# Kernel tuning notes

Measured on AMD Instinct MI355X. Metric: run time of the kernel, lower is better.

The kernel has to match this reference:

```python
import jax, jax.numpy as jnp
import numpy as np

B, L, D = 64, 2048, 256
T_CLAIM, T_PREM = 16, 32
NEG = jnp.float32(-1e9)


def setup_inputs() -> dict:
    key = jax.random.key(0)
    ks = jax.random.split(key, 40)
    f32 = jnp.float32

    def n(k, shape, scale):
        return jax.random.normal(k, shape, f32) * scale

    inp = {}
    inp["sentence_feat"] = n(ks[0], (B, L, D), 1.0)
    inp["sentence_mask"] = jnp.ones((B, L), jnp.int32)
    inp["gold_claim_head"] = jax.random.randint(ks[1], (B, T_CLAIM), 0, L, jnp.int32)
    inp["gold_premise_head"] = jax.random.randint(ks[2], (B, T_PREM), 0, L, jnp.int32)
    inp["query_claim"] = n(ks[3], (D,), 1.0)
    inp["query_premise"] = n(ks[4], (D,), 1.0)
    s = D ** -0.5
    for px, kb in (("c_", 5), ("p_", 20)):
        inp[px + "bil_W"] = n(ks[kb + 0], (D, D, D), 1.0 / D)   # (out,in1,in2)
        inp[px + "bil_b"] = jnp.zeros((D,), f32)
        inp[px + "Wq"] = n(ks[kb + 1], (D, D), s)
        inp[px + "Wk"] = n(ks[kb + 2], (D, D), s)
        inp[px + "attn_b"] = jnp.zeros((D,), f32)
        inp[px + "attn_v"] = n(ks[kb + 3], (D,), s)
        inp[px + "Wih"] = n(ks[kb + 4], (3 * D, D), s)
        inp[px + "Whh"] = n(ks[kb + 5], (3 * D, D), s)
        inp[px + "bih"] = jnp.zeros((3 * D,), f32)
        inp[px + "bhh"] = jnp.zeros((3 * D,), f32)
    return inp


def _gru_cell(x, h, Wih, Whh, bih, bhh):
    # torch.nn.GRUCell math
    gi = x @ Wih.T + bih
    gh = h @ Whh.T + bhh
    ir, iz, in_ = jnp.split(gi, 3, axis=-1)
    hr, hz, hn = jnp.split(gh, 3, axis=-1)
    r = jax.nn.sigmoid(ir + hr)
    z = jax.nn.sigmoid(iz + hz)
    nn_ = jnp.tanh(in_ + r * hn)
    return (1.0 - z) * nn_ + z * h


def _pointer_network(parent, sib0, emb, mask, gold,
                     bil_W, bil_b, Wq, Wk, attn_b, attn_v, Wih, Whh, bih, bhh):
    """parent (B,D), sib0 (B,D), emb (B,L,D), mask (B,L), gold (B,T) -> (B,T) gold probs."""
    bidx = jnp.arange(parent.shape[0])
    proj_k = jnp.einsum('bld,de->ble', emb, Wk)  # key projection hoisted out of loop
    valid = mask != 0

    def step(sib, gold_t):
        # bilinear query: q_k = parent W_k sib + b_k
        q = jnp.einsum('bd,kde,be->bk', parent, bil_W, sib) + bil_b  # (B,D)
        h = jnp.tanh(proj_k + (q @ Wq + attn_b)[:, None, :])          # (B,L,D)
        scores = jnp.einsum('bld,d->bl', h, attn_v)                   # (B,L)
        prob = jax.nn.softmax(jnp.where(valid, scores, NEG), axis=-1)
        tp = prob[bidx, gold_t]                                       # gather gold prob
        x = emb[bidx, gold_t]                                         # gather gold embedding
        return _gru_cell(x, sib, Wih, Whh, bih, bhh), tp

    _, probs = jax.lax.scan(step, sib0, gold.T)  # (T,B)
    return probs.T


def reference(sentence_feat, query_claim, query_premise,
              c_bil_W, c_bil_b, c_Wq, c_Wk, c_attn_b, c_attn_v, c_Wih, c_Whh, c_bih, c_bhh,
              p_bil_W, p_bil_b, p_Wq, p_Wk, p_attn_b, p_attn_v, p_Wih, p_Whh, p_bih, p_bhh,
              sentence_mask, gold_claim_head, gold_premise_head):
    global_feat = sentence_feat[:, -2]                       # (B,D)
    sib_c = jnp.broadcast_to(query_claim, global_feat.shape)
    sib_p = jnp.broadcast_to(query_premise, global_feat.shape)
    claim = _pointer_network(global_feat, sib_c, sentence_feat, sentence_mask, gold_claim_head,
                             c_bil_W, c_bil_b, c_Wq, c_Wk, c_attn_b, c_attn_v, c_Wih, c_Whh, c_bih, c_bhh)
    prem = _pointer_network(global_feat, sib_p, sentence_feat, sentence_mask, gold_premise_head,
                            p_bil_W, p_bil_b, p_Wq, p_Wk, p_attn_b, p_attn_v, p_Wih, p_Whh, p_bih, p_bhh)
    return claim, prem
```

## Files before the change

kernel.cpp:

```cpp
#include <hip/hip_runtime.h>
#include <hip/hip_fp16.h>

#define B_ 64
#define L_ 2048
#define D_ 256
#define TC 16
#define TP 32

typedef _Float16 half8 __attribute__((ext_vector_type(8)));
typedef _Float16 f16x2 __attribute__((ext_vector_type(2)));
typedef float f32x4 __attribute__((ext_vector_type(4)));

#define LOG2E 1.4426950408889634f
#define TWO_LOG2E 2.8853900817779268f

__device__ __forceinline__ float ex2(float x){ return __builtin_amdgcn_exp2f(x); }
__device__ __forceinline__ float rcp_(float x){ return __builtin_amdgcn_rcpf(x); }
__device__ __forceinline__ float sigm(float x){ return rcp_(1.f + ex2(-LOG2E*x)); }
__device__ __forceinline__ float tanh_(float x){ return 1.f - 2.f*rcp_(1.f + ex2(TWO_LOG2E*x)); }

#if __has_builtin(__builtin_amdgcn_fdot2)
__device__ __forceinline__ float fdot2_(f16x2 a, f16x2 b, float c){ return __builtin_amdgcn_fdot2(a,b,c,false); }
#else
__device__ __forceinline__ float fdot2_(f16x2 a, f16x2 b, float c){
  return fmaf((float)a[0], (float)b[0], fmaf((float)a[1], (float)b[1], c));
}
#endif

__device__ __forceinline__ void cvt8(uint4 v, float* w){
  const __half2* h = (const __half2*)&v;
#pragma unroll
  for (int i=0;i<4;i++){ float2 f = __half22float2(h[i]); w[2*i]=f.x; w[2*i+1]=f.y; }
}

__global__ __launch_bounds__(256) void k_prep(
    const float* __restrict__ sf,
    const float* __restrict__ wk_c, const float* __restrict__ wk_p,
    const float* __restrict__ wih_c, const float* __restrict__ wih_p,
    const float* __restrict__ whh_c, const float* __restrict__ whh_p,
    __half* __restrict__ wkT, __half* __restrict__ wihH, __half* __restrict__ whhH,
    float* __restrict__ parentT)
{
  int idx = blockIdx.x*256 + threadIdx.x;
  if (idx < 131072) {
    int c = idx >> 8, d = idx & 255;
    int net = c >> 8, e = c & 255;
    const float* w = net ? wk_p : wk_c;
    wkT[idx] = __float2half(w[d*256 + e]);
  } else if (idx < 131072 + 393216) {
    int i = idx - 131072;
    const float* w = (i < 196608) ? wih_c : wih_p;
    wihH[i] = __float2half(w[(i < 196608) ? i : i - 196608]);
  } else if (idx < 131072 + 786432) {
    int i = idx - 131072 - 393216;
    const float* w = (i < 196608) ? whh_c : whh_p;
    whhH[i] = __float2half(w[(i < 196608) ? i : i - 196608]);
  } else {
    int i = idx - 131072 - 786432;
    int d = i >> 6, b = i & 63;
    parentT[i] = sf[((size_t)b*L_ + (L_-2))*D_ + d];
  }
}

__global__ __launch_bounds__(256) void k_gemm(
    const float* __restrict__ sf, const __half* __restrict__ wkT, __half* __restrict__ Eo)
{
  __shared__ __half As[128*40];
  __shared__ __half Bs[128*40];
  const int tid = threadIdx.x;
  const int bid = blockIdx.x;
  const int xcd = bid & 7;
  const int w_  = bid >> 3;
  const int row0 = (xcd*128 + (w_ >> 2)) * 128;
  const int col0 = (w_ & 3) * 128;
  const int lane = tid & 63, wave = tid >> 6;
  const int wm = wave & 1, wn = wave >> 1;
  const int qd = lane >> 4, mr = lane & 15;
  const int rl = tid >> 1, hf = tid & 1;

  f32x4 acc[4][4];
#pragma unroll
  for (int i=0;i<4;i++)
#pragma unroll
    for (int j=0;j<4;j++) acc[i][j] = (f32x4){0.f,0.f,0.f,0.f};

  for (int kc = 0; kc < 256; kc += 32) {
    const float* asrc = sf + ((size_t)(row0+rl))*256 + kc + hf*16;
    __half* adst = As + rl*40 + hf*16;
#pragma unroll
    for (int i=0;i<4;i++){
      float4 v = ((const float4*)asrc)[i];
      __half2 h01 = __floats2half2_rn(v.x, v.y);
      __half2 h23 = __floats2half2_rn(v.z, v.w);
      uint2 u; u.x = *(const unsigned*)&h01; u.y = *(const unsigned*)&h23;
      *(uint2*)(adst + i*4) = u;
    }
    const __half* bsrc = wkT + (size_t)(col0+rl)*256 + kc + hf*16;
    __half* bdst = Bs + rl*40 + hf*16;
    *(uint4*)bdst       = *(const uint4*)bsrc;
    *(uint4*)(bdst + 8) = *(const uint4*)(bsrc + 8);
    __syncthreads();

    half8 af[4], bf[4];
#pragma unroll
    for (int tm=0;tm<4;tm++) af[tm] = *(const half8*)(As + (wm*64 + tm*16 + mr)*40 + qd*8);
#pragma unroll
    for (int tn=0;tn<4;tn++) bf[tn] = *(const half8*)(Bs + (wn*64 + tn*16 + mr)*40 + qd*8);
#pragma unroll
    for (int tm=0;tm<4;tm++)
#pragma unroll
      for (int tn=0;tn<4;tn++)
        acc[tm][tn] = __builtin_amdgcn_mfma_f32_16x16x32_f16(af[tm], bf[tn], acc[tm][tn], 0,0,0);
    __syncthreads();
  }
#pragma unroll
  for (int tm=0;tm<4;tm++)
#pragma unroll
    for (int tn=0;tn<4;tn++){
      int c = col0 + wn*64 + tn*16 + mr;
#pragma unroll
      for (int rg=0; rg<4; rg++){
        int r = row0 + wm*64 + tm*16 + qd*4 + rg;
        float e = ex2(TWO_LOG2E * acc[tm][tn][rg]);
        Eo[(size_t)r*512 + c] = __float2half(fminf(e, 65000.f));
      }
    }
}

__global__ __launch_bounds__(256) void k_M(
    const float* __restrict__ bw_c, const float* __restrict__ bw_p,
    const float* __restrict__ parentT, float* __restrict__ M)
{
  const int net = blockIdx.x >> 8;
  const int k = blockIdx.x & 255;
  const int e = threadIdx.x;
  __shared__ float pl[16384];
#pragma unroll
  for (int r=0;r<16;r++){
    int f4 = r*256 + threadIdx.x;
    ((float4*)pl)[f4] = ((const float4*)parentT)[f4];
  }
  __syncthreads();

  const float* W = (net ? bw_p : bw_c) + (size_t)k*65536 + e;
  float acc[64];
#pragma unroll
  for (int b=0;b<64;b++) acc[b] = 0.f;
  float wcur = W[0];
  for (int d=0; d<256; d++){
    float wnext = (d < 255) ? W[(size_t)(d+1)*256] : 0.f;
    const float4* pr = (const float4*)(pl + d*64);
#pragma unroll
    for (int c=0;c<16;c++){
      float4 pv = pr[c];
      acc[c*4+0] = fmaf(pv.x, wcur, acc[c*4+0]);
      acc[c*4+1] = fmaf(pv.y, wcur, acc[c*4+1]);
      acc[c*4+2] = fmaf(pv.z, wcur, acc[c*4+2]);
      acc[c*4+3] = fmaf(pv.w, wcur, acc[c*4+3]);
    }
    wcur = wnext;
  }
  float* Mo = M + ((size_t)net*64*256 + k)*256 + e;
#pragma unroll
  for (int b=0;b<64;b++) Mo[(size_t)b*65536] = acc[b];
}

template<int T>
__global__ __launch_bounds__(256) void k_gi(
    const float* __restrict__ sf, const int* __restrict__ gold,
    const __half* __restrict__ wih, const float* __restrict__ bih,
    float* __restrict__ gi_all)
{
  const int jc = blockIdx.x % 3;
  const int bb = blockIdx.x / 3;
  __shared__ float xs[T-1][256];
  const int* gr = gold + bb*T;
  for (int t=0; t<T-1; t++)
    xs[t][threadIdx.x] = sf[((size_t)bb*L_ + gr[t])*D_ + threadIdx.x];
  __syncthreads();
  const int j = jc*256 + threadIdx.x;
  const __half* wr = wih + (size_t)j*256;
  float acc[T-1];
#pragma unroll
  for (int t=0;t<T-1;t++) acc[t] = 0.f;
  for (int d0=0; d0<256; d0+=8){
    uint4 wv = *(const uint4*)(wr + d0);
    float w[8]; cvt8(wv, w);
#pragma unroll
    for (int t=0;t<T-1;t++){
      const float* xr = &xs[t][d0];
      float4 a = *(const float4*)xr;
      float4 b = *(const float4*)(xr+4);
      acc[t] += w[0]*a.x + w[1]*a.y + w[2]*a.z + w[3]*a.w
              + w[4]*b.x + w[5]*b.y + w[6]*b.z + w[7]*b.w;
    }
  }
  float bias = bih[j];
  float* go = gi_all + ((size_t)bb*32)*768 + j;
#pragma unroll
  for (int t=0;t<T-1;t++) go[(size_t)t*768] = acc[t] + bias;
}

__global__ __launch_bounds__(768, 3) void k_gru(
    const float* __restrict__ query_c, const float* __restrict__ query_p,
    const __half* __restrict__ whhH,
    const float* __restrict__ bhh_c, const float* __restrict__ bhh_p,
    const float* __restrict__ gi_all, float* __restrict__ sibT)
{
  const int net = blockIdx.x >> 6, bb = blockIdx.x & 63;
  const int T = net ? TP : TC;
  const int j = threadIdx.x;
  __shared__ float hs[256];
  __shared__ __half hsh[256];
  __shared__ float gh[768];
  const __half* wr = whhH + (size_t)net*196608 + (size_t)j*256;
  const float bias = (net ? bhh_p : bhh_c)[j];
  const float* gir = gi_all + (size_t)(net*64+bb)*32*768;
  float* sib = sibT + (size_t)(net*64+bb)*256*32;
  const float* query = net ? query_p : query_c;

  uint4 wreg[32];
#pragma unroll
  for (int i=0;i<32;i++) wreg[i] = ((const uint4*)wr)[i];

  if (j < 256){ float h0 = query[j]; hs[j]=h0; hsh[j]=__float2half(h0); sib[j*32]=h0; }
  __syncthreads();
  for (int t=0; t<T-1; t++){
    float a0 = bias, a1 = 0.f, a2 = 0.f, a3 = 0.f;
#pragma unroll
    for (int i=0;i<32;i+=4){
      uint4 hv0 = ((const uint4*)hsh)[i+0];
      uint4 hv1 = ((const uint4*)hsh)[i+1];
      uint4 hv2 = ((const uint4*)hsh)[i+2];
      uint4 hv3 = ((const uint4*)hsh)[i+3];
      const f16x2* wp0 = (const f16x2*)&wreg[i+0]; const f16x2* hp0 = (const f16x2*)&hv0;
      const f16x2* wp1 = (const f16x2*)&wreg[i+1]; const f16x2* hp1 = (const f16x2*)&hv1;
      const f16x2* wp2 = (const f16x2*)&wreg[i+2]; const f16x2* hp2 = (const f16x2*)&hv2;
      const f16x2* wp3 = (const f16x2*)&wreg[i+3]; const f16x2* hp3 = (const f16x2*)&hv3;
#pragma unroll
      for (int i2=0;i2<4;i2++){
        a0 = fdot2_(wp0[i2], hp0[i2], a0);
        a1 = fdot2_(wp1[i2], hp1[i2], a1);
        a2 = fdot2_(wp2[i2], hp2[i2], a2);
        a3 = fdot2_(wp3[i2], hp3[i2], a3);
      }
    }
    gh[j] = (a0 + a1) + (a2 + a3);
    __syncthreads();
    if (j < 256){
      const float* gi = gir + (size_t)t*768;
      float r = sigm(gi[j] + gh[j]);
      float z = sigm(gi[256+j] + gh[256+j]);
      float n = tanh_(gi[512+j] + r*gh[512+j]);
      float hn = (1.f - z)*n + z*hs[j];
      hs[j] = hn; hsh[j] = __float2half(hn);
      sib[j*32 + t + 1] = hn;
    }
    __syncthreads();
  }
}

__global__ __launch_bounds__(256) void k_qt(
    const float* __restrict__ M, const float* __restrict__ sibT,
    const float* __restrict__ bb_c, const float* __restrict__ bb_p,
    const float* __restrict__ wq_c, const float* __restrict__ wq_p,
    const float* __restrict__ ab_c, const float* __restrict__ ab_p,
    float* __restrict__ Qo)
{
  const int bb = blockIdx.x;
  const int y = blockIdx.y;
  const int net = (y >= 2) ? 1 : 0;
  const int t0 = net ? (y-2)*8 : y*8;
  const int tid = threadIdx.x;
  __shared__ float qs[256][8];
  __shared__ float slds[256][8];

  {
    const float* sr = sibT + ((size_t)(net*64+bb))*256*32 + t0;
#pragma unroll
    for (int r=0;r<2;r++){
      int f4 = r*256 + tid;
      int e = f4 >> 1, hh = f4 & 1;
      *(float4*)&slds[e][hh*4] = *(const float4*)(sr + (size_t)e*32 + hh*4);
    }
  }
  __syncthreads();

  const float* Mr = M + (((size_t)(net*64+bb))*256 + tid)*256;
  float accq[8];
  const float b0 = (net ? bb_p : bb_c)[tid];
#pragma unroll
  for (int t=0;t<8;t++) accq[t] = b0;
  for (int e0=0; e0<256; e0+=4){
    float4 m4 = *(const float4*)(Mr + e0);
#pragma unroll
    for (int ee=0; ee<4; ee++){
      float4 sa = *(const float4*)&slds[e0+ee][0];
      float4 sb = *(const float4*)&slds[e0+ee][4];
      float mv = ((const float*)&m4)[ee];
      accq[0] = fmaf(mv, sa.x, accq[0]); accq[1] = fmaf(mv, sa.y, accq[1]);
      accq[2] = fmaf(mv, sa.z, accq[2]); accq[3] = fmaf(mv, sa.w, accq[3]);
      accq[4] = fmaf(mv, sb.x, accq[4]); accq[5] = fmaf(mv, sb.y, accq[5]);
      accq[6] = fmaf(mv, sb.z, accq[6]); accq[7] = fmaf(mv, sb.w, accq[7]);
    }
  }
#pragma unroll
  for (int t=0;t<8;t++) qs[tid][t] = accq[t];
  __syncthreads();

  const float* wq = (net ? wq_p : wq_c) + tid;
  float acc2[8];
  const float a0 = (net ? ab_p : ab_c)[tid];
#pragma unroll
  for (int t=0;t<8;t++) acc2[t] = a0;
  for (int k=0; k<256; k++){
    float w = wq[(size_t)k*256];
#pragma unroll
    for (int t=0;t<8;t++) acc2[t] = fmaf(qs[k][t], w, acc2[t]);
  }
  float* qo = Qo + (((size_t)(net*64+bb))*256 + tid)*32 + t0;
#pragma unroll
  for (int t=0;t<8;t++) qo[t] = fminf(ex2(TWO_LOG2E * acc2[t]), 3.0e4f);
}

__global__ __launch_bounds__(256) void k_fused(
    const __half* __restrict__ E, const float* __restrict__ Q,
    const float* __restrict__ av_c, const float* __restrict__ av_p,
    const int* __restrict__ mask,
    const int* __restrict__ gold_c, const int* __restrict__ gold_p,
    float* __restrict__ partials, float* __restrict__ gold_e)
{
  const int bb = blockIdx.x;
  const int lc = blockIdx.y;
  const int nc = blockIdx.z;
  const int net = nc ? 1 : 0;
  const int t0 = (nc == 2) ? 16 : 0;
  const int l  = lc*256 + threadIdx.x;
  const __half* pr = E + ((size_t)bb*L_ + l)*512 + net*256;
  const float* qr = Q + ((size_t)(net*64+bb))*256*32 + t0;
  const float* av = net ? av_p : av_c;

  float acc[16];
#pragma unroll
  for (int t=0;t<16;t++) acc[t] = 0.f;

  for (int d0=0; d0<256; d0+=8){
    uint4 pv = *(const uint4*)(pr + d0);
    float x[8]; cvt8(pv, x);
#pragma unroll
    for (int h=0; h<2; h++){
      const int d = d0 + h*4;
      const float v0 = av[d+0], v1 = av[d+1], v2 = av[d+2], v3 = av[d+3];
      const float xa = x[h*4+0], xb = x[h*4+1], xc = x[h*4+2], xd = x[h*4+3];
      const float* q0p = qr + (size_t)(d+0)*32;
      const float* q1p = qr + (size_t)(d+1)*32;
      const float* q2p = qr + (size_t)(d+2)*32;
      const float* q3p = qr + (size_t)(d+3)*32;
#pragma unroll
      for (int tc=0; tc<16; tc+=4){
        float4 qa  = *(const float4*)(q0p + tc);
        float4 qb  = *(const float4*)(q1p + tc);
        float4 qc  = *(const float4*)(q2p + tc);
        float4 qd4 = *(const float4*)(q3p + tc);
        const float qas[4] = {qa.x, qa.y, qa.z, qa.w};
        const float qbs[4] = {qb.x, qb.y, qb.z, qb.w};
        const float qcs[4] = {qc.x, qc.y, qc.z, qc.w};
        const float qds[4] = {qd4.x,qd4.y,qd4.z,qd4.w};
#pragma unroll
        for (int tt=0; tt<4; tt++){
          float ta = fmaf(xa, qas[tt], 1.f);
          float tb = fmaf(xb, qbs[tt], 1.f);
          float tcv= fmaf(xc, qcs[tt], 1.f);
          float td = fmaf(xd, qds[tt], 1.f);
          float t01 = ta*tb, t23 = tcv*td;
          float n01 = fmaf(v0, tb, v1*ta);
          float n23 = fmaf(v2, td, v3*tcv);
          float num = fmaf(n01, t23, n23*t01);
          float den = t01*t23;
          acc[tc+tt] = fmaf(num, rcp_(den), acc[tc+tt]);
        }
      }
    }
  }

  const int m = mask[bb*L_ + l];
  float ex[16];
#pragma unroll
  for (int t=0;t<16;t++) ex[t] = m ? ex2(-TWO_LOG2E * acc[t]) : 0.f;

  const int* g = net ? (gold_p + bb*TP + t0) : (gold_c + bb*TC);
#pragma unroll
  for (int t=0;t<16;t++)
    if (l == g[t]) gold_e[net*2048 + bb*32 + t0 + t] = ex[t];

#pragma unroll
  for (int off=1; off<64; off<<=1)
#pragma unroll
    for (int t=0;t<16;t++) ex[t] += __shfl_xor(ex[t], off, 64);

  __shared__ float red4[4][16];
  const int lane = threadIdx.x & 63, wave = threadIdx.x >> 6;
  if (lane == 0)
#pragma unroll
    for (int t=0;t<16;t++) red4[wave][t] = ex[t];
  __syncthreads();
  if (threadIdx.x < 16){
    float s = red4[0][threadIdx.x] + red4[1][threadIdx.x]
            + red4[2][threadIdx.x] + red4[3][threadIdx.x];
    partials[(((size_t)nc*64 + bb)*8 + lc)*16 + threadIdx.x] = s;
  }
}

__global__ __launch_bounds__(256) void k_fin(
    const float* __restrict__ partials, const float* __restrict__ gold_e,
    float* __restrict__ out)
{
  int id = blockIdx.x*256 + threadIdx.x;
  if (id >= 3072) return;
  int net, bb, t, nc, tt;
  if (id < 1024){ net=0; bb=id>>4; t=id&15; nc=0; tt=t; }
  else { int i=id-1024; net=1; bb=i>>5; t=i&31; nc=1+(t>>4); tt=t&15; }
  const float* pr = partials + (((size_t)nc*64 + bb)*8)*16 + tt;
  float s = 0.f;
#pragma unroll
  for (int lcx=0; lcx<8; lcx++) s += pr[lcx*16];
  out[net ? (1024 + bb*TP + t) : (bb*TC + t)] = gold_e[net*2048 + bb*32 + t] / s;
}

extern "C" void kernel_launch(void* const* d_in, const int* in_sizes, int n_in,
                              void* d_out, int out_size, void* d_ws, size_t ws_size,
                              hipStream_t stream)
{
  const float* sf      = (const float*)d_in[0];
  const int*   mask    = (const int*)d_in[1];
  const int*   gold_c  = (const int*)d_in[2];
  const int*   gold_p  = (const int*)d_in[3];
  const float* query_c = (const float*)d_in[4];
  const float* query_p = (const float*)d_in[5];
  const float* c_bw  = (const float*)d_in[6];
  const float* c_bb  = (const float*)d_in[7];
  const float* c_wq  = (const float*)d_in[8];
  const float* c_wk  = (const float*)d_in[9];
  const float* c_ab  = (const float*)d_in[10];
  const float* c_av  = (const float*)d_in[11];
  const float* c_wih = (const float*)d_in[12];
  const float* c_whh = (const float*)d_in[13];
  const float* c_bih = (const float*)d_in[14];
  const float* c_bhh = (const float*)d_in[15];
  const float* p_bw  = (const float*)d_in[16];
  const float* p_bb  = (const float*)d_in[17];
  const float* p_wq  = (const float*)d_in[18];
  const float* p_wk  = (const float*)d_in[19];
  const float* p_ab  = (const float*)d_in[20];
  const float* p_av  = (const float*)d_in[21];
  const float* p_wih = (const float*)d_in[22];
  const float* p_whh = (const float*)d_in[23];
  const float* p_bih = (const float*)d_in[24];
  const float* p_bhh = (const float*)d_in[25];
  float* out = (float*)d_out;

  char* w = (char*)d_ws;
  size_t o = 0;
  auto take = [&](size_t bytes){ char* p = w + o; o += (bytes + 255) & ~(size_t)255; return p; };
  __half* E      = (__half*)take((size_t)131072*512*2);
  float*  M      = (float*) take((size_t)2*64*256*256*4);
  float*  Q      = (float*) take((size_t)2*64*256*32*4);
  float*  sibT   = (float*) take((size_t)2*64*256*32*4);
  float*  gi_all = (float*) take((size_t)2*64*32*768*4);
  float*  partials=(float*) take((size_t)3*64*8*16*4);
  float*  gold_e = (float*) take((size_t)2*64*32*4);
  __half* wkT    = (__half*)take((size_t)512*256*2);
  __half* wihH   = (__half*)take((size_t)2*768*256*2);
  __half* whhH   = (__half*)take((size_t)2*768*256*2);
  float*  parentT= (float*) take((size_t)256*64*4);
  (void)ws_size; (void)in_sizes; (void)n_in; (void)out_size;

  k_prep<<<3648, 256, 0, stream>>>(sf, c_wk, p_wk, c_wih, p_wih, c_whh, p_whh,
                                   wkT, wihH, whhH, parentT);
  k_gemm<<<4096, 256, 0, stream>>>(sf, wkT, E);
  k_M<<<512, 256, 0, stream>>>(c_bw, p_bw, parentT, M);
  k_gi<TC><<<192, 256, 0, stream>>>(sf, gold_c, wihH,          c_bih, gi_all);
  k_gi<TP><<<192, 256, 0, stream>>>(sf, gold_p, wihH + 196608, p_bih, gi_all + (size_t)64*32*768);
  k_gru<<<128, 768, 0, stream>>>(query_c, query_p, whhH, c_bhh, p_bhh, gi_all, sibT);
  k_qt<<<dim3(64,6), 256, 0, stream>>>(M, sibT, c_bb, p_bb, c_wq, p_wq, c_ab, p_ab, Q);
  k_fused<<<dim3(64,8,3), 256, 0, stream>>>(E, Q, c_av, p_av, mask, gold_c, gold_p,
                                            partials, gold_e);
  k_fin<<<12, 256, 0, stream>>>(partials, gold_e, out);
}
```

Baseline: 763.0 us.

## Merge M/gi kernels, drop Wih fp16 conversion, restructure premise scoring split

Merges the bilinear M kernel and both GRU input-gate kernels into one launch, and removes the Wih fp16 conversion so gi reads fp32 weights directly. Rewrites the scoring kernel so each premise thread covers all 32 timesteps over half of D, with the two halves combined through shared memory. This reuses each loaded E element across twice as many timesteps, and the E loads are software-prefetched. The cost is higher register pressure (32 accumulators plus the ex array) and an extra block-level reduction.

```diff
diff --git a/kernel.cpp b/kernel.cpp
--- a/kernel.cpp
+++ b/kernel.cpp
@@ -33,12 +33,51 @@
   for (int i=0;i<4;i++){ float2 f = __half22float2(h[i]); w[2*i]=f.x; w[2*i+1]=f.y; }
 }
 
+template<int NT>
+__device__ __forceinline__ void octet_body(const float* x, const float* av_d,
+                                           const float* qr_d, float* acc)
+{
+#pragma unroll
+  for (int h=0; h<2; h++){
+    const int d = h*4;
+    const float v0 = av_d[d+0], v1 = av_d[d+1], v2 = av_d[d+2], v3 = av_d[d+3];
+    const float xa = x[h*4+0], xb = x[h*4+1], xc = x[h*4+2], xd = x[h*4+3];
+    const float* q0p = qr_d + (size_t)(d+0)*32;
+    const float* q1p = qr_d + (size_t)(d+1)*32;
+    const float* q2p = qr_d + (size_t)(d+2)*32;
+    const float* q3p = qr_d + (size_t)(d+3)*32;
+#pragma unroll
+    for (int tc=0; tc<NT; tc+=4){
+      float4 qa  = *(const float4*)(q0p + tc);
+      float4 qb  = *(const float4*)(q1p + tc);
+      float4 qc  = *(const float4*)(q2p + tc);
+      float4 qd4 = *(const float4*)(q3p + tc);
+      const float qas[4] = {qa.x, qa.y, qa.z, qa.w};
+      const float qbs[4] = {qb.x, qb.y, qb.z, qb.w};
+      const float qcs[4] = {qc.x, qc.y, qc.z, qc.w};
+      const float qds[4] = {qd4.x,qd4.y,qd4.z,qd4.w};
+#pragma unroll
+      for (int tt=0; tt<4; tt++){
+        float ta = fmaf(xa, qas[tt], 1.f);
+        float tb = fmaf(xb, qbs[tt], 1.f);
+        float tcv= fmaf(xc, qcs[tt], 1.f);
+        float td = fmaf(xd, qds[tt], 1.f);
+        float t01 = ta*tb, t23 = tcv*td;
+        float n01 = fmaf(v0, tb, v1*ta);
+        float n23 = fmaf(v2, td, v3*tcv);
+        float num = fmaf(n01, t23, n23*t01);
+        float den = t01*t23;
+        acc[tc+tt] = fmaf(num, rcp_(den), acc[tc+tt]);
+      }
+    }
+  }
+}
+
 __global__ __launch_bounds__(256) void k_prep(
     const float* __restrict__ sf,
     const float* __restrict__ wk_c, const float* __restrict__ wk_p,
-    const float* __restrict__ wih_c, const float* __restrict__ wih_p,
     const float* __restrict__ whh_c, const float* __restrict__ whh_p,
-    __half* __restrict__ wkT, __half* __restrict__ wihH, __half* __restrict__ whhH,
+    __half* __restrict__ wkT, __half* __restrict__ whhH,
     float* __restrict__ parentT)
 {
   int idx = blockIdx.x*256 + threadIdx.x;
@@ -49,14 +88,10 @@
     wkT[idx] = __float2half(w[d*256 + e]);
   } else if (idx < 131072 + 393216) {
     int i = idx - 131072;
-    const float* w = (i < 196608) ? wih_c : wih_p;
-    wihH[i] = __float2half(w[(i < 196608) ? i : i - 196608]);
-  } else if (idx < 131072 + 786432) {
-    int i = idx - 131072 - 393216;
     const float* w = (i < 196608) ? whh_c : whh_p;
     whhH[i] = __float2half(w[(i < 196608) ? i : i - 196608]);
   } else {
-    int i = idx - 131072 - 786432;
+    int i = idx - 524288;
     int d = i >> 6, b = i & 63;
     parentT[i] = sf[((size_t)b*L_ + (L_-2))*D_ + d];
   }
@@ -127,65 +162,27 @@
     }
 }
 
-__global__ __launch_bounds__(256) void k_M(
-    const float* __restrict__ bw_c, const float* __restrict__ bw_p,
-    const float* __restrict__ parentT, float* __restrict__ M)
-{
-  const int net = blockIdx.x >> 8;
-  const int k = blockIdx.x & 255;
-  const int e = threadIdx.x;
-  __shared__ float pl[16384];
-#pragma unroll
-  for (int r=0;r<16;r++){
-    int f4 = r*256 + threadIdx.x;
-    ((float4*)pl)[f4] = ((const float4*)parentT)[f4];
-  }
-  __syncthreads();
-
-  const float* W = (net ? bw_p : bw_c) + (size_t)k*65536 + e;
-  float acc[64];
-#pragma unroll
-  for (int b=0;b<64;b++) acc[b] = 0.f;
-  float wcur = W[0];
-  for (int d=0; d<256; d++){
-    float wnext = (d < 255) ? W[(size_t)(d+1)*256] : 0.f;
-    const float4* pr = (const float4*)(pl + d*64);
-#pragma unroll
-    for (int c=0;c<16;c++){
-      float4 pv = pr[c];
-      acc[c*4+0] = fmaf(pv.x, wcur, acc[c*4+0]);
-      acc[c*4+1] = fmaf(pv.y, wcur, acc[c*4+1]);
-      acc[c*4+2] = fmaf(pv.z, wcur, acc[c*4+2]);
-      acc[c*4+3] = fmaf(pv.w, wcur, acc[c*4+3]);
-    }
-    wcur = wnext;
-  }
-  float* Mo = M + ((size_t)net*64*256 + k)*256 + e;
-#pragma unroll
-  for (int b=0;b<64;b++) Mo[(size_t)b*65536] = acc[b];
-}
-
 template<int T>
-__global__ __launch_bounds__(256) void k_gi(
-    const float* __restrict__ sf, const int* __restrict__ gold,
-    const __half* __restrict__ wih, const float* __restrict__ bih,
-    float* __restrict__ gi_all)
-{
-  const int jc = blockIdx.x % 3;
-  const int bb = blockIdx.x / 3;
-  __shared__ float xs[T-1][256];
+__device__ void gi_body(const float* __restrict__ sf, const int* __restrict__ gold,
+                        const float* __restrict__ wih, const float* __restrict__ bih,
+                        float* __restrict__ gi_out, int idx, float* xsm)
+{
+  const int jc = idx % 3;
+  const int bb = idx / 3;
+  float (*xs)[256] = (float(*)[256])xsm;
   const int* gr = gold + bb*T;
   for (int t=0; t<T-1; t++)
     xs[t][threadIdx.x] = sf[((size_t)bb*L_ + gr[t])*D_ + threadIdx.x];
   __syncthreads();
   const int j = jc*256 + threadIdx.x;
-  const __half* wr = wih + (size_t)j*256;
+  const float* wr = wih + (size_t)j*256;
   float acc[T-1];
 #pragma unroll
   for (int t=0;t<T-1;t++) acc[t] = 0.f;
   for (int d0=0; d0<256; d0+=8){
-    uint4 wv = *(const uint4*)(wr + d0);
-    float w[8]; cvt8(wv, w);
+    float4 wa = *(const float4*)(wr + d0);
+    float4 wb = *(const float4*)(wr + d0 + 4);
+    const float w[8] = {wa.x,wa.y,wa.z,wa.w, wb.x,wb.y,wb.z,wb.w};
 #pragma unroll
     for (int t=0;t<T-1;t++){
       const float* xr = &xs[t][d0];
@@ -196,9 +193,60 @@
     }
   }
   float bias = bih[j];
-  float* go = gi_all + ((size_t)bb*32)*768 + j;
+  float* go = gi_out + ((size_t)bb*32)*768 + j;
 #pragma unroll
   for (int t=0;t<T-1;t++) go[(size_t)t*768] = acc[t] + bias;
+}
+
+__global__ __launch_bounds__(256) void k_Mgi(
+    const float* __restrict__ bw_c, const float* __restrict__ bw_p,
+    const float* __restrict__ parentT, float* __restrict__ M,
+    const float* __restrict__ sf,
+    const int* __restrict__ gold_c, const int* __restrict__ gold_p,
+    const float* __restrict__ wih_c, const float* __restrict__ wih_p,
+    const float* __restrict__ bih_c, const float* __restrict__ bih_p,
+    float* __restrict__ gi_all)
+{
+  __shared__ float smem[16384];
+  const int bid = blockIdx.x;
+  if (bid < 512) {
+    const int net = bid >> 8;
+    const int k = bid & 255;
+    const int e = threadIdx.x;
+    float* pl = smem;
+#pragma unroll
+    for (int r=0;r<16;r++){
+      int f4 = r*256 + threadIdx.x;
+      ((float4*)pl)[f4] = ((const float4*)parentT)[f4];
+    }
+    __syncthreads();
+
+    const float* W = (net ? bw_p : bw_c) + (size_t)k*65536 + e;
+    float acc[64];
+#pragma unroll
+    for (int b=0;b<64;b++) acc[b] = 0.f;
+    float wcur = W[0];
+    for (int d=0; d<256; d++){
+      float wnext = (d < 255) ? W[(size_t)(d+1)*256] : 0.f;
+      const float4* pr = (const float4*)(pl + d*64);
+#pragma unroll
+      for (int c=0;c<16;c++){
+        float4 pv = pr[c];
+        acc[c*4+0] = fmaf(pv.x, wcur, acc[c*4+0]);
+        acc[c*4+1] = fmaf(pv.y, wcur, acc[c*4+1]);
+        acc[c*4+2] = fmaf(pv.z, wcur, acc[c*4+2]);
+        acc[c*4+3] = fmaf(pv.w, wcur, acc[c*4+3]);
+      }
+      wcur = wnext;
+    }
+    float* Mo = M + ((size_t)net*64*256 + k)*256 + e;
+#pragma unroll
+    for (int b=0;b<64;b++) Mo[(size_t)b*65536] = acc[b];
+  } else if (bid < 704) {
+    gi_body<TC>(sf, gold_c, wih_c, bih_c, gi_all, bid-512, smem);
+  } else {
+    gi_body<TP>(sf, gold_p, wih_p, bih_p, gi_all + (size_t)64*32*768, bid-704, smem);
+  }
 }
 
 __global__ __launch_bounds__(768, 3) void k_gru(
@@ -323,108 +371,147 @@
   for (int t=0;t<8;t++) qo[t] = fminf(ex2(TWO_LOG2E * acc2[t]), 3.0e4f);
 }
 
-__global__ __launch_bounds__(256) void k_fused(
+__global__ __launch_bounds__(256) void k_fused2(
     const __half* __restrict__ E, const float* __restrict__ Q,
     const float* __restrict__ av_c, const float* __restrict__ av_p,
     const int* __restrict__ mask,
     const int* __restrict__ gold_c, const int* __restrict__ gold_p,
-    float* __restrict__ partials, float* __restrict__ gold_e)
+    float* __restrict__ partials_c, float* __restrict__ partials_p,
+    float* __restrict__ gold_e)
 {
   const int bb = blockIdx.x;
-  const int lc = blockIdx.y;
-  const int nc = blockIdx.z;
-  const int net = nc ? 1 : 0;
-  const int t0 = (nc == 2) ? 16 : 0;
-  const int l  = lc*256 + threadIdx.x;
-  const __half* pr = E + ((size_t)bb*L_ + l)*512 + net*256;
-  const float* qr = Q + ((size_t)(net*64+bb))*256*32 + t0;
-  const float* av = net ? av_p : av_c;
-
-  float acc[16];
-#pragma unroll
-  for (int t=0;t<16;t++) acc[t] = 0.f;
-
-  for (int d0=0; d0<256; d0+=8){
-    uint4 pv = *(const uint4*)(pr + d0);
-    float x[8]; cvt8(pv, x);
-#pragma unroll
-    for (int h=0; h<2; h++){
-      const int d = d0 + h*4;
-      const float v0 = av[d+0], v1 = av[d+1], v2 = av[d+2], v3 = av[d+3];
-      const float xa = x[h*4+0], xb = x[h*4+1], xc = x[h*4+2], xd = x[h*4+3];
-      const float* q0p = qr + (size_t)(d+0)*32;
-      const float* q1p = qr + (size_t)(d+1)*32;
-      const float* q2p = qr + (size_t)(d+2)*32;
-      const float* q3p = qr + (size_t)(d+3)*32;
-#pragma unroll
-      for (int tc=0; tc<16; tc+=4){
-        float4 qa  = *(const float4*)(q0p + tc);
-        float4 qb  = *(const float4*)(q1p + tc);
-        float4 qc  = *(const float4*)(q2p + tc);
-        float4 qd4 = *(const float4*)(q3p + tc);
-        const float qas[4] = {qa.x, qa.y, qa.z, qa.w};
-        const float qbs[4] = {qb.x, qb.y, qb.z, qb.w};
-        const float qcs[4] = {qc.x, qc.y, qc.z, qc.w};
-        const float qds[4] = {qd4.x,qd4.y,qd4.z,qd4.w};
-#pragma unroll
-        for (int tt=0; tt<4; tt++){
-          float ta = fmaf(xa, qas[tt], 1.f);
-          float tb = fmaf(xb, qbs[tt], 1.f);
-          float tcv= fmaf(xc, qcs[tt], 1.f);
-          float td = fmaf(xd, qds[tt], 1.f);
-          float t01 = ta*tb, t23 = tcv*td;
-          float n01 = fmaf(v0, tb, v1*ta);
-          float n23 = fmaf(v2, td, v3*tcv);
-          float num = fmaf(n01, t23, n23*t01);
-          float den = t01*t23;
-          acc[tc+tt] = fmaf(num, rcp_(den), acc[tc+tt]);
-        }
+  const int y  = blockIdx.y;
+  const int tid = threadIdx.x;
+  const int lane = tid & 63, wave = tid >> 6;
+  __shared__ float redP[128][32];
+  __shared__ float red2[2][32];
+
+  if (y < 8) {
+    const int lc = y;
+    const int l  = lc*256 + tid;
+    const __half* pr = E + ((size_t)bb*L_ + l)*512;
+    const float* qr = Q + ((size_t)bb)*256*32;
+    const float* av = av_c;
+
+    float acc[16];
+#pragma unroll
+    for (int t=0;t<16;t++) acc[t] = 0.f;
+
+    const uint4* e4 = (const uint4*)pr;
+    uint4 pv = e4[0];
+    for (int o=0; o<32; o++){
+      uint4 nx = e4[(o<31)?(o+1):31];
+      float x[8]; cvt8(pv, x);
+      const int d0 = o*8;
+      octet_body<16>(x, av + d0, qr + (size_t)d0*32, acc);
+      pv = nx;
+    }
+
+    const int m = mask[bb*L_ + l];
+    float ex[16];
+#pragma unroll
+    for (int t=0;t<16;t++) ex[t] = m ? ex2(-TWO_LOG2E * acc[t]) : 0.f;
+
+    const int* g = gold_c + bb*TC;
+#pragma unroll
+    for (int t=0;t<16;t++)
+      if (l == g[t]) gold_e[bb*32 + t] = ex[t];
+
+#pragma unroll
+    for (int off=1; off<64; off<<=1)
+#pragma unroll
+      for (int t=0;t<16;t++) ex[t] += __shfl_xor(ex[t], off, 64);
+
+    if (lane == 0)
+#pragma unroll
+      for (int t=0;t<16;t++) redP[wave][t] = ex[t];
+    __syncthreads();
+    if (tid < 16){
+      float s = redP[0][tid] + redP[1][tid] + redP[2][tid] + redP[3][tid];
+      partials_c[((size_t)bb*8 + lc)*16 + tid] = s;
+    }
+  } else {
+    const int lc = y - 8;
+    const int lloc = tid & 127, hh = tid >> 7;
+    const int l = lc*128 + lloc;
+    const __half* pr = E + ((size_t)bb*L_ + l)*512 + 256 + hh*128;
+    const float* qr = Q + ((size_t)(64+bb)*256 + hh*128)*32;
+    const float* av = av_p + hh*128;
+
+    float acc[32];
+#pragma unroll
+    for (int t=0;t<32;t++) acc[t] = 0.f;
+
+    const uint4* e4 = (const uint4*)pr;
+    uint4 pv = e4[0];
+    for (int o=0; o<16; o++){
+      uint4 nx = e4[(o<15)?(o+1):15];
+      float x[8]; cvt8(pv, x);
+      const int d0 = o*8;
+      octet_body<32>(x, av + d0, qr + (size_t)d0*32, acc);
+      pv = nx;
+    }
+
+    if (hh == 1){
+#pragma unroll
+      for (int t=0;t<32;t++) redP[lloc][t] = acc[t];
+    }
+    __syncthreads();
+
+    float ex[32];
+#pragma unroll
+    for (int t=0;t<32;t++) ex[t] = 0.f;
+    if (hh == 0){
+      const int m = mask[bb*L_ + l];
+      const int* g = gold_p + bb*TP;
+#pragma unroll
+      for (int t=0;t<32;t++){
+        float a = acc[t] + redP[lloc][t];
+        ex[t] = m ? ex2(-TWO_LOG2E * a) : 0.f;
       }
-    }
-  }
-
-  const int m = mask[bb*L_ + l];
-  float ex[16];
-#pragma unroll
-  for (int t=0;t<16;t++) ex[t] = m ? ex2(-TWO_LOG2E * acc[t]) : 0.f;
-
-  const int* g = net ? (gold_p + bb*TP + t0) : (gold_c + bb*TC);
-#pragma unroll
-  for (int t=0;t<16;t++)
-    if (l == g[t]) gold_e[net*2048 + bb*32 + t0 + t] = ex[t];
-
-#pragma unroll
-  for (int off=1; off<64; off<<=1)
-#pragma unroll
-    for (int t=0;t<16;t++) ex[t] += __shfl_xor(ex[t], off, 64);
-
-  __shared__ float red4[4][16];
-  const int lane = threadIdx.x & 63, wave = threadIdx.x >> 6;
-  if (lane == 0)
-#pragma unroll
-    for (int t=0;t<16;t++) red4[wave][t] = ex[t];
-  __syncthreads();
-  if (threadIdx.x < 16){
-    float s = red4[0][threadIdx.x] + red4[1][threadIdx.x]
-            + red4[2][threadIdx.x] + red4[3][threadIdx.x];
-    partials[(((size_t)nc*64 + bb)*8 + lc)*16 + threadIdx.x] = s;
+#pragma unroll
+      for (int t=0;t<32;t++)
+        if (l == g[t]) gold_e[2048 + bb*32 + t] = ex[t];
+    }
+
+#pragma unroll
+    for (int off=1; off<64; off<<=1)
+#pragma unroll
+      for (int t=0;t<32;t++) ex[t] += __shfl_xor(ex[t], off, 64);
+
+    if (hh == 0 && lane == 0)
+#pragma unroll
+      for (int t=0;t<32;t++) red2[wave][t] = ex[t];
+    __syncthreads();
+    if (tid < 32){
+      float s = red2[0][tid] + red2[1][tid];
+      partials_p[((size_t)bb*16 + lc)*32 + tid] = s;
+    }
   }
 }
 
 __global__ __launch_bounds__(256) void k_fin(
-    const float* __restrict__ partials, const float* __restrict__ gold_e,
-    float* __restrict__ out)
+    const float* __restrict__ partials_c, const float* __restrict__ partials_p,
+    const float* __restrict__ gold_e, float* __restrict__ out)
 {
   int id = blockIdx.x*256 + threadIdx.x;
   if (id >= 3072) return;
-  int net, bb, t, nc, tt;
-  if (id < 1024){ net=0; bb=id>>4; t=id&15; nc=0; tt=t; }
-  else { int i=id-1024; net=1; bb=i>>5; t=i&31; nc=1+(t>>4); tt=t&15; }
-  const float* pr = partials + (((size_t)nc*64 + bb)*8)*16 + tt;
-  float s = 0.f;
-#pragma unroll
-  for (int lcx=0; lcx<8; lcx++) s += pr[lcx*16];
-  out[net ? (1024 + bb*TP + t) : (bb*TC + t)] = gold_e[net*2048 + bb*32 + t] / s;
+  if (id < 1024){
+    int bb = id >> 4, t = id & 15;
+    const float* pr = partials_c + ((size_t)bb*8)*16 + t;
+    float s = 0.f;
+#pragma unroll
+    for (int lcx=0; lcx<8; lcx++) s += pr[lcx*16];
+    out[bb*TC + t] = gold_e[bb*32 + t] / s;
+  } else {
+    int i = id - 1024;
+    int bb = i >> 5, t = i & 31;
+    const float* pr = partials_p + ((size_t)bb*16)*32 + t;
+    float s = 0.f;
+#pragma unroll
+    for (int lcx=0; lcx<16; lcx++) s += pr[lcx*32];
+    out[1024 + bb*TP + t] = gold_e[2048 + bb*32 + t] / s;
+  }
 }
 
 extern "C" void kernel_launch(void* const* d_in, const int* in_sizes, int n_in,
@@ -462,28 +549,26 @@
   char* w = (char*)d_ws;
   size_t o = 0;
   auto take = [&](size_t bytes){ char* p = w + o; o += (bytes + 255) & ~(size_t)255; return p; };
-  __half* E      = (__half*)take((size_t)131072*512*2);
-  float*  M      = (float*) take((size_t)2*64*256*256*4);
-  float*  Q      = (float*) take((size_t)2*64*256*32*4);
-  float*  sibT   = (float*) take((size_t)2*64*256*32*4);
-  float*  gi_all = (float*) take((size_t)2*64*32*768*4);
-  float*  partials=(float*) take((size_t)3*64*8*16*4);
-  float*  gold_e = (float*) take((size_t)2*64*32*4);
-  __half* wkT    = (__half*)take((size_t)512*256*2);
-  __half* wihH   = (__half*)take((size_t)2*768*256*2);
-  __half* whhH   = (__half*)take((size_t)2*768*256*2);
-  float*  parentT= (float*) take((size_t)256*64*4);
+  __half* E       = (__half*)take((size_t)131072*512*2);
+  float*  M       = (float*) take((size_t)2*64*256*256*4);
+  float*  Q       = (float*) take((size_t)2*64*256*32*4);
+  float*  sibT    = (float*) take((size_t)2*64*256*32*4);
+  float*  gi_all  = (float*) take((size_t)2*64*32*768*4);
+  float*  partials_c = (float*) take((size_t)64*8*16*4);
+  float*  partials_p = (float*) take((size_t)64*16*32*4);
+  float*  gold_e  = (float*) take((size_t)2*64*32*4);
+  __half* wkT     = (__half*)take((size_t)512*256*2);
+  __half* whhH    = (__half*)take((size_t)2*768*256*2);
+  float*  parentT = (float*) take((size_t)256*64*4);
   (void)ws_size; (void)in_sizes; (void)n_in; (void)out_size;
 
-  k_prep<<<3648, 256, 0, stream>>>(sf, c_wk, p_wk, c_wih, p_wih, c_whh, p_whh,
-                                   wkT, wihH, whhH, parentT);
+  k_prep<<<2112, 256, 0, stream>>>(sf, c_wk, p_wk, c_whh, p_whh, wkT, whhH, parentT);
   k_gemm<<<4096, 256, 0, stream>>>(sf, wkT, E);
-  k_M<<<512, 256, 0, stream>>>(c_bw, p_bw, parentT, M);
-  k_gi<TC><<<192, 256, 0, stream>>>(sf, gold_c, wihH,          c_bih, gi_all);
-  k_gi<TP><<<192, 256, 0, stream>>>(sf, gold_p, wihH + 196608, p_bih, gi_all + (size_t)64*32*768);
+  k_Mgi<<<896, 256, 0, stream>>>(c_bw, p_bw, parentT, M, sf, gold_c, gold_p,
+                                 c_wih, p_wih, c_bih, p_bih, gi_all);
   k_gru<<<128, 768, 0, stream>>>(query_c, query_p, whhH, c_bhh, p_bhh, gi_all, sibT);
   k_qt<<<dim3(64,6), 256, 0, stream>>>(M, sibT, c_bb, p_bb, c_wq, p_wq, c_ab, p_ab, Q);
-  k_fused<<<dim3(64,8,3), 256, 0, stream>>>(E, Q, c_av, p_av, mask, gold_c, gold_p,
-                                            partials, gold_e);
-  k_fin<<<12, 256, 0, stream>>>(partials, gold_e, out);
-}
+  k_fused2<<<dim3(64,24), 256, 0, stream>>>(E, Q, c_av, p_av, mask, gold_c, gold_p,
+                                            partials_c, partials_p, gold_e);
+  k_fin<<<12, 256, 0, stream>>>(partials_c, partials_p, gold_e, out);
+}
```

After: 856.0 us. 12.2% more time.
